# Kernel tuning notes

Measured on AMD Instinct MI355X. Metric: run time of the kernel, lower is better.

## Reference

```python
import jax, jax.numpy as jnp
import numpy as np


def setup_inputs() -> dict:
    key = jax.random.key(0)
    k1, k2, k3, k4 = jax.random.split(key, 4)
    N, T, F = 8192, 128, 9
    M_s = 256
    merged = jax.random.normal(k1, (N, T, F), dtype=jnp.float32)
    input1 = jax.random.normal(k2, (N, T, F), dtype=jnp.float32)
    samples = jax.random.normal(k3, (N, M_s), dtype=jnp.float32)
    labels = jax.random.randint(k4, (N,), 0, 10, dtype=jnp.int32)
    return {"merged": merged, "input1": input1, "samples": samples, "labels": labels}


def reference(merged, input1, samples, labels):
    # Pairwise squared distances S_ij = sum_k (s_i - s_j)^2 / M_s, computed via
    # the Gram-matrix identity instead of materializing the [N, N, M_s] tensor.
    M_s = samples.shape[1]
    sq = jnp.sum(samples * samples, axis=-1)                 # [N]
    gram = jnp.einsum('im,jm->ij', samples, samples)         # [N, N]
    S_ij = (sq[:, None] + sq[None, :] - 2.0 * gram) / jnp.float32(M_s)
    same = (labels[:, None] == labels[None, :]).astype(jnp.float32)
    term2 = jnp.mean(jnp.maximum(0.0, (1.0 - same) * (1.0 - S_ij)))
    L_label = 10.0 * jnp.mean(same * S_ij) + 10.0 * term2
    return L_label
```

## Files before the change

kernel.cpp:

```cpp
#include <hip/hip_runtime.h>

#define NROWS 8192
#define KDIM  256
#define NT    64
#define NBLK  (NT * (NT + 1) / 2)
#define GRID  512

typedef __attribute__((ext_vector_type(4)))  float f32x4;
typedef __attribute__((ext_vector_type(16))) float f32x16;
typedef __attribute__((ext_vector_type(4)))  int   i32x4;
typedef __attribute__((ext_vector_type(8)))  int   i32x8;

#define GLD(gp, lp)                                                            \
  __builtin_amdgcn_global_load_lds(                                            \
      (const __attribute__((address_space(1))) void*)(gp),                     \
      (__attribute__((address_space(3))) void*)(lp), 16, 0, 0)

__global__ __launch_bounds__(256) void prep_kernel(
    const float* __restrict__ samples, const int* __restrict__ labels,
    unsigned char* __restrict__ sf8, float2* __restrict__ meta,
    float* __restrict__ out) {
  int tid = blockIdx.x * 256 + threadIdx.x;
  int gw = tid >> 6;
  int lane = tid & 63;
#pragma unroll
  for (int it = 0; it < NROWS / 1024; ++it) {
    int row = gw + it * 1024;
    f32x4 v = ((const f32x4*)samples)[(size_t)row * 64 + lane];
    int pk = __builtin_amdgcn_cvt_pk_fp8_f32(v.x, v.y, 0, false);
    pk = __builtin_amdgcn_cvt_pk_fp8_f32(v.z, v.w, pk, true);
    ((unsigned int*)sf8)[(size_t)row * 64 + lane] = (unsigned int)pk;
    float p = v.x * v.x + v.y * v.y + v.z * v.z + v.w * v.w;
#pragma unroll
    for (int off = 32; off; off >>= 1) p += __shfl_down(p, off);
    if (lane == 0)
      meta[row] = make_float2(p * (1.0f / 256.0f), (float)labels[row]);
  }
  if (tid == 0) out[0] = 0.0f;
}

__device__ inline void decode_tile(int b, int& bi, int& bj) {
  float disc = (2.0f * NT + 1.0f) * (2.0f * NT + 1.0f) - 8.0f * (float)b;
  bi = (int)(((2.0f * NT + 1.0f) - sqrtf(disc)) * 0.5f);
  if (bi < 0) bi = 0;
  if (bi > NT - 1) bi = NT - 1;
  while (bi > 0 && (bi * NT - bi * (bi - 1) / 2) > b) --bi;
  while (((bi + 1) * NT - (bi + 1) * bi / 2) <= b) ++bi;
  bj = bi + (b - (bi * NT - bi * (bi - 1) / 2));
}

__global__ __launch_bounds__(512, 2) void pair_kernel(
    const unsigned char* __restrict__ sf8, const float2* __restrict__ meta,
    float* __restrict__ out) {

  __shared__ __align__(16) unsigned char As[128 * 256];
  __shared__ __align__(16) unsigned char Bs[128 * 256];
  __shared__ float red[8];

  int t = threadIdx.x;
  int lane = t & 63;
  int w = t >> 6;
  int wm = w >> 1, wn = w & 1;
  int lr = lane >> 4, pc = lane & 15;
  int l31 = lane & 31;
  int hk  = lane >> 5;

  float stt = 0.f;

  auto stage = [&](int bi_, int bj_) {
    int rA = bi_ * 128, rB = bj_ * 128;
#pragma unroll
    for (int p = 0; p < 4; ++p) {
      int region = p * 8 + w;
      int rr = region * 4 + lr;
      int c = pc ^ (rr & 15);
      GLD(sf8 + (size_t)(rA + rr) * KDIM + c * 16, &As[region * 1024]);
      GLD(sf8 + (size_t)(rB + rr) * KDIM + c * 16, &Bs[region * 1024]);
    }
  };

  int tile = blockIdx.x;
  int bi, bj;

  while (tile < NBLK) {
    decode_tile(tile, bi, bj);

    stage(bi, bj);

    float sqa[16], laa[16], sqb[2], labv[2];
#pragma unroll
    for (int g = 0; g < 4; ++g) {
      int gr = bi * 128 + wm * 32 + g * 8 + 4 * hk;
      f32x4 m0 = *(const f32x4*)(meta + gr);
      f32x4 m1 = *(const f32x4*)(meta + gr + 2);
      sqa[g * 4 + 0] = m0.x; laa[g * 4 + 0] = m0.y;
      sqa[g * 4 + 1] = m0.z; laa[g * 4 + 1] = m0.w;
      sqa[g * 4 + 2] = m1.x; laa[g * 4 + 2] = m1.y;
      sqa[g * 4 + 3] = m1.z; laa[g * 4 + 3] = m1.w;
    }
#pragma unroll
    for (int j = 0; j < 2; ++j) {
      float2 mb = meta[bj * 128 + wn * 64 + j * 32 + l31];
      sqb[j] = mb.x; labv[j] = mb.y;
    }
    float wt = (bi == bj) ? 1.0f : 2.0f;

    __syncthreads();

    f32x16 acc[2];
#pragma unroll
    for (int j = 0; j < 2; ++j)
#pragma unroll
      for (int e = 0; e < 16; ++e) acc[j][e] = 0.f;

    int m = wm * 32 + l31;
    const unsigned char* ab = &As[m * 256];
    int sm = m & 15;
#pragma unroll
    for (int kt = 0; kt < 4; ++kt) {
      int c0 = kt * 4 + hk * 2;
      i32x4 alo = *(const i32x4*)(ab + ((c0 ^ sm) << 4));
      i32x4 ahi = *(const i32x4*)(ab + (((c0 + 1) ^ sm) << 4));
      i32x8 av = {alo.x, alo.y, alo.z, alo.w, ahi.x, ahi.y, ahi.z, ahi.w};
#pragma unroll
      for (int j = 0; j < 2; ++j) {
        int n = wn * 64 + j * 32 + l31;
        const unsigned char* bb = &Bs[n * 256];
        int sn = n & 15;
        i32x4 blo = *(const i32x4*)(bb + ((c0 ^ sn) << 4));
        i32x4 bhi = *(const i32x4*)(bb + (((c0 + 1) ^ sn) << 4));
        i32x8 bv = {blo.x, blo.y, blo.z, blo.w, bhi.x, bhi.y, bhi.z, bhi.w};
        acc[j] = __builtin_amdgcn_mfma_scale_f32_32x32x64_f8f6f4(
            av, bv, acc[j], 0, 0, 0, 127, 0, 127);
      }
    }

    float s = 0.f;
#pragma unroll
    for (int j = 0; j < 2; ++j) {
#pragma unroll
      for (int g2 = 0; g2 < 16; ++g2) {
        float S = sqa[g2] + sqb[j] - acc[j][g2] * (1.0f / 128.0f);
        float h = fmaxf(0.f, 1.f - S);
        s += (laa[g2] == labv[j]) ? S : h;
      }
    }
    stt += wt * s;

    tile += GRID;
    if (tile < NBLK) __syncthreads();
  }

#pragma unroll
  for (int off = 32; off; off >>= 1) stt += __shfl_down(stt, off);
  if (lane == 0) red[w] = stt;
  __syncthreads();
  if (t == 0) {
    float a = 0.f;
#pragma unroll
    for (int q = 0; q < 8; q++) a += red[q];
    atomicAdd(&out[0], a * (10.0f / ((float)NROWS * (float)NROWS)));
  }
}

extern "C" void kernel_launch(void* const* d_in, const int* in_sizes, int n_in,
                              void* d_out, int out_size, void* d_ws,
                              size_t ws_size, hipStream_t stream) {
  const float* samples = (const float*)d_in[2];
  const int*   labels  = (const int*)d_in[3];

  char* ws = (char*)d_ws;
  unsigned char* sf8 = (unsigned char*)ws;
  float2* meta = (float2*)(ws + (size_t)NROWS * KDIM);
  float* out   = (float*)d_out;

  prep_kernel<<<256, 256, 0, stream>>>(samples, labels, sf8, meta, out);
  pair_kernel<<<GRID, 512, 0, stream>>>(sf8, meta, out);
}
```

Baseline: 129.1 us.

## Split K into two LDS halves and prefetch next tile's first half

The 256-wide K dimension is now staged in two 128-byte halves in separate LDS buffers. The second half is loaded while MFMAs run on the first half. The next tile's first half is prefetched while MFMAs run on the current second half. This hides global-to-LDS load latency behind compute, in exchange for an extra barrier per tile and a swizzle over 8 chunks instead of 16. The LDS footprint stays the same.

```diff
diff --git a/kernel.cpp b/kernel.cpp
--- a/kernel.cpp
+++ b/kernel.cpp
@@ -53,39 +53,75 @@
     const unsigned char* __restrict__ sf8, const float2* __restrict__ meta,
     float* __restrict__ out) {
 
-  __shared__ __align__(16) unsigned char As[128 * 256];
-  __shared__ __align__(16) unsigned char Bs[128 * 256];
+  __shared__ __align__(16) unsigned char As[2][128 * 128];
+  __shared__ __align__(16) unsigned char Bs[2][128 * 128];
   __shared__ float red[8];
 
   int t = threadIdx.x;
   int lane = t & 63;
   int w = t >> 6;
   int wm = w >> 1, wn = w & 1;
-  int lr = lane >> 4, pc = lane & 15;
+  int lr = lane >> 3, pc = lane & 7;
   int l31 = lane & 31;
   int hk  = lane >> 5;
 
   float stt = 0.f;
 
-  auto stage = [&](int bi_, int bj_) {
-    int rA = bi_ * 128, rB = bj_ * 128;
-#pragma unroll
-    for (int p = 0; p < 4; ++p) {
+  auto stageA = [&](int bi_, int ck) {
+    int rA = bi_ * 128;
+#pragma unroll
+    for (int p = 0; p < 2; ++p) {
       int region = p * 8 + w;
-      int rr = region * 4 + lr;
-      int c = pc ^ (rr & 15);
-      GLD(sf8 + (size_t)(rA + rr) * KDIM + c * 16, &As[region * 1024]);
-      GLD(sf8 + (size_t)(rB + rr) * KDIM + c * 16, &Bs[region * 1024]);
+      int rr = region * 8 + lr;
+      int c = pc ^ (rr & 7);
+      GLD(sf8 + (size_t)(rA + rr) * KDIM + ck * 128 + c * 16,
+          &As[ck][region * 1024]);
+    }
+  };
+  auto stageB = [&](int bj_, int ck) {
+    int rB = bj_ * 128;
+#pragma unroll
+    for (int p = 0; p < 2; ++p) {
+      int region = p * 8 + w;
+      int rr = region * 8 + lr;
+      int c = pc ^ (rr & 7);
+      GLD(sf8 + (size_t)(rB + rr) * KDIM + ck * 128 + c * 16,
+          &Bs[ck][region * 1024]);
+    }
+  };
+
+  auto domfma = [&](f32x16 (&acc)[2], int ck) {
+    int m = wm * 32 + l31;
+    const unsigned char* ab = &As[ck][m * 128];
+    int sm = m & 7;
+#pragma unroll
+    for (int kt = 0; kt < 2; ++kt) {
+      int c0 = kt * 4 + hk * 2;
+      i32x4 alo = *(const i32x4*)(ab + ((c0 ^ sm) << 4));
+      i32x4 ahi = *(const i32x4*)(ab + (((c0 + 1) ^ sm) << 4));
+      i32x8 av = {alo.x, alo.y, alo.z, alo.w, ahi.x, ahi.y, ahi.z, ahi.w};
+#pragma unroll
+      for (int j = 0; j < 2; ++j) {
+        int n = wn * 64 + j * 32 + l31;
+        const unsigned char* bb = &Bs[ck][n * 128];
+        int sn = n & 7;
+        i32x4 blo = *(const i32x4*)(bb + ((c0 ^ sn) << 4));
+        i32x4 bhi = *(const i32x4*)(bb + (((c0 + 1) ^ sn) << 4));
+        i32x8 bv = {blo.x, blo.y, blo.z, blo.w, bhi.x, bhi.y, bhi.z, bhi.w};
+        acc[j] = __builtin_amdgcn_mfma_scale_f32_32x32x64_f8f6f4(
+            av, bv, acc[j], 0, 0, 0, 127, 0, 127);
+      }
     }
   };
 
   int tile = blockIdx.x;
   int bi, bj;
+  decode_tile(tile, bi, bj);
+  stageA(bi, 0);
+  stageB(bj, 0);
 
   while (tile < NBLK) {
-    decode_tile(tile, bi, bj);
-
-    stage(bi, bj);
+    __syncthreads();
 
     float sqa[16], laa[16], sqb[2], labv[2];
 #pragma unroll
@@ -105,35 +141,29 @@
     }
     float wt = (bi == bj) ? 1.0f : 2.0f;
 
+    stageA(bi, 1);
+    stageB(bj, 1);
+
+    f32x16 acc[2];
+#pragma unroll
+    for (int j = 0; j < 2; ++j)
+#pragma unroll
+      for (int e = 0; e < 16; ++e) acc[j][e] = 0.f;
+
+    domfma(acc, 0);
+
     __syncthreads();
 
-    f32x16 acc[2];
-#pragma unroll
-    for (int j = 0; j < 2; ++j)
-#pragma unroll
-      for (int e = 0; e < 16; ++e) acc[j][e] = 0.f;
-
-    int m = wm * 32 + l31;
-    const unsigned char* ab = &As[m * 256];
-    int sm = m & 15;
-#pragma unroll
-    for (int kt = 0; kt < 4; ++kt) {
-      int c0 = kt * 4 + hk * 2;
-      i32x4 alo = *(const i32x4*)(ab + ((c0 ^ sm) << 4));
-      i32x4 ahi = *(const i32x4*)(ab + (((c0 + 1) ^ sm) << 4));
-      i32x8 av = {alo.x, alo.y, alo.z, alo.w, ahi.x, ahi.y, ahi.z, ahi.w};
-#pragma unroll
-      for (int j = 0; j < 2; ++j) {
-        int n = wn * 64 + j * 32 + l31;
-        const unsigned char* bb = &Bs[n * 256];
-        int sn = n & 15;
-        i32x4 blo = *(const i32x4*)(bb + ((c0 ^ sn) << 4));
-        i32x4 bhi = *(const i32x4*)(bb + (((c0 + 1) ^ sn) << 4));
-        i32x8 bv = {blo.x, blo.y, blo.z, blo.w, bhi.x, bhi.y, bhi.z, bhi.w};
-        acc[j] = __builtin_amdgcn_mfma_scale_f32_32x32x64_f8f6f4(
-            av, bv, acc[j], 0, 0, 0, 127, 0, 127);
-      }
-    }
+    int ntile = tile + GRID;
+    int nbi = 0, nbj = 0;
+    bool have_next = ntile < NBLK;
+    if (have_next) {
+      decode_tile(ntile, nbi, nbj);
+      stageA(nbi, 0);
+      stageB(nbj, 0);
+    }
+
+    domfma(acc, 1);
 
     float s = 0.f;
 #pragma unroll
@@ -147,8 +177,7 @@
     }
     stt += wt * s;
 
-    tile += GRID;
-    if (tile < NBLK) __syncthreads();
+    tile = ntile; bi = nbi; bj = nbj;
   }
 
 #pragma unroll
```

Measured after the change: 128.5 us. Within noise of the previous version (-0.4%).
